# Optimization experiments

Measured on AMD Instinct MI355X. Metric: run time of the kernel, lower is better.

The kernel has to match this reference:

```python
import jax, jax.numpy as jnp
import numpy as np

N_HEADS = 32
N_KV_HEADS = 8
HEAD_DIM = 64  # dim // n_heads = 2048 // 32

def setup_inputs() -> dict:
    key = jax.random.key(0)
    k1, k2, k3, k4, k5 = jax.random.split(key, 5)
    B, T, D = 2, 2048, 2048
    s = 0.02
    return {
        "x": jax.random.normal(k1, (B, T, D), dtype=jnp.float32),
        "wq": jax.random.normal(k2, (D, D), dtype=jnp.float32) * s,
        "wk": jax.random.normal(k3, (N_KV_HEADS * HEAD_DIM, D), dtype=jnp.float32) * s,
        "wv": jax.random.normal(k4, (N_KV_HEADS * HEAD_DIM, D), dtype=jnp.float32) * s,
        "wo": jax.random.normal(k5, (D, D), dtype=jnp.float32) * s,
    }

def reference(x, wq, wk, wv, wo):
    B, T, D = x.shape
    ratio = N_HEADS // N_KV_HEADS
    scale = HEAD_DIM ** -0.5
    # projections (nn.Linear: x @ W.T)
    q = (x @ wq.T).reshape(B, T, N_HEADS, HEAD_DIM)
    k = (x @ wk.T).reshape(B, T, N_KV_HEADS, HEAD_DIM)
    v = (x @ wv.T).reshape(B, T, N_KV_HEADS, HEAD_DIM)
    # GQA expand: [B,T,kvh,d] -> [B,T,kvh*ratio,d]
    k = jnp.broadcast_to(k[:, :, :, None, :], (B, T, N_KV_HEADS, ratio, HEAD_DIM)).reshape(B, T, N_HEADS, HEAD_DIM)
    v = jnp.broadcast_to(v[:, :, :, None, :], (B, T, N_KV_HEADS, ratio, HEAD_DIM)).reshape(B, T, N_HEADS, HEAD_DIM)
    # [B,H,T,d]
    q = q.transpose(0, 2, 1, 3)
    k = k.transpose(0, 2, 1, 3)
    v = v.transpose(0, 2, 1, 3)
    # naive full score matrix [B,H,T,T]
    score = jnp.einsum('bhqd,bhkd->bhqk', q, k) * scale
    causal = jnp.triu(jnp.full((T, T), -jnp.inf, dtype=score.dtype), k=1)
    score = score + causal
    # upcast to fp32 for softmax (matches score.float())
    attn = jax.nn.softmax(score.astype(jnp.float32), axis=-1)
    out = jnp.einsum('bhqk,bhkd->bhqd', attn, v.astype(jnp.float32)).astype(x.dtype)
    out = out.transpose(0, 2, 1, 3).reshape(B, T, N_HEADS * HEAD_DIM)
    return out @ wo.T
```

## Files before the change

### kernel.cpp

```cpp
#include <hip/hip_runtime.h>
#include <hip/hip_bf16.h>

typedef unsigned short u16;
typedef unsigned int   u32;
typedef __attribute__((ext_vector_type(8))) short s16x8;
typedef __attribute__((ext_vector_type(4))) float f32x4;

__device__ __forceinline__ u16 f2bf(float f) {
    u32 u = __float_as_uint(f);
    u += 0x7fff + ((u >> 16) & 1);
    return (u16)(u >> 16);
}

__device__ __forceinline__ u16 f2bf_fast(float f) {
    __hip_bfloat16 h = __float2bfloat16(f);
    return *reinterpret_cast<u16*>(&h);
}

__device__ __forceinline__ f32x4 mfma16(s16x8 a, s16x8 b, f32x4 c) {
    return __builtin_amdgcn_mfma_f32_16x16x32_bf16(a, b, c, 0, 0, 0);
}

#define GLL16(g, l)                                                            \
    __builtin_amdgcn_global_load_lds(                                          \
        (const __attribute__((address_space(1))) void*)(g),                    \
        (__attribute__((address_space(3))) void*)(l), 16, 0, 0)

__global__ void cvt_f32_bf16(const float* __restrict__ src, u16* __restrict__ dst, int n8) {
    int i = blockIdx.x * blockDim.x + threadIdx.x;
    if (i >= n8) return;
    const float4* s4 = reinterpret_cast<const float4*>(src);
    float4 a = s4[2 * i], b = s4[2 * i + 1];
    s16x8 o;
    o[0] = (short)f2bf(a.x); o[1] = (short)f2bf(a.y);
    o[2] = (short)f2bf(a.z); o[3] = (short)f2bf(a.w);
    o[4] = (short)f2bf(b.x); o[5] = (short)f2bf(b.y);
    o[6] = (short)f2bf(b.z); o[7] = (short)f2bf(b.w);
    reinterpret_cast<s16x8*>(dst)[i] = o;
}

__global__ void cvt_weights(const float* __restrict__ wq, const float* __restrict__ wk,
                            const float* __restrict__ wv, const float* __restrict__ wo,
                            u16* __restrict__ wqkv, u16* __restrict__ wob) {
    int i = blockIdx.x * blockDim.x + threadIdx.x;
    const float* src; u16* dst;
    if (i < 524288)       { src = wq + (size_t)i * 8;            dst = wqkv + (size_t)i * 8; }
    else if (i < 655360)  { int j = i - 524288; src = wk + (size_t)j * 8; dst = wqkv + 4194304 + (size_t)j * 8; }
    else if (i < 786432)  { int j = i - 655360; src = wv + (size_t)j * 8; dst = wqkv + 5242880 + (size_t)j * 8; }
    else                  { int j = i - 786432; src = wo + (size_t)j * 8; dst = wob + (size_t)j * 8; }
    const float4* s4 = reinterpret_cast<const float4*>(src);
    float4 a = s4[0], b = s4[1];
    s16x8 o;
    o[0] = (short)f2bf(a.x); o[1] = (short)f2bf(a.y);
    o[2] = (short)f2bf(a.z); o[3] = (short)f2bf(a.w);
    o[4] = (short)f2bf(b.x); o[5] = (short)f2bf(b.y);
    o[6] = (short)f2bf(b.z); o[7] = (short)f2bf(b.w);
    *reinterpret_cast<s16x8*>(dst) = o;
}

template <int BF16_OUT>
__global__ __launch_bounds__(256, 3)
void gemm_bt(const u16* __restrict__ A, const u16* __restrict__ B,
             void* __restrict__ Cout, int M, int N, int K, int nbx) {
    const int nwg = gridDim.x;
    const int cpx = nwg >> 3;
    const int swz = (blockIdx.x & 7) * cpx + (blockIdx.x >> 3);
    const int by = swz / nbx, bx = swz - by * nbx;
    __shared__ __align__(16) u16 As[128 * 32];
    __shared__ __align__(16) u16 Bs[128 * 32];
    const int tid = threadIdx.x;
    const int w = tid >> 6, ln = tid & 63;
    const int m0 = by * 128, n0 = bx * 128;
    const int wr = w >> 1, wc = w & 1;
    const int g = ln >> 4, c15 = ln & 15;
    f32x4 acc[4][4] = {};
    const int srow0 = w * 32 + (ln >> 2);
    const int spos = ln & 3;
    for (int k0 = 0; k0 < K; k0 += 32) {
        __syncthreads();
#pragma unroll
        for (int j = 0; j < 2; ++j) {
            int row = srow0 + j * 16;
            int ch = spos ^ ((row >> 1) & 3);
            const u16* ga = A + (size_t)(m0 + row) * K + k0 + ch * 8;
            GLL16(ga, (char*)As + (w * 32 + j * 16) * 64);
            const u16* gb = B + (size_t)(n0 + row) * K + k0 + ch * 8;
            GLL16(gb, (char*)Bs + (w * 32 + j * 16) * 64);
        }
        __syncthreads();
        s16x8 af[4], bfr[4];
#pragma unroll
        for (int ms = 0; ms < 4; ++ms) {
            int row = wr * 64 + ms * 16 + c15;
            int cp = g ^ ((row >> 1) & 3);
            af[ms] = *reinterpret_cast<const s16x8*>((const char*)As + row * 64 + cp * 16);
        }
#pragma unroll
        for (int ns = 0; ns < 4; ++ns) {
            int row = wc * 64 + ns * 16 + c15;
            int cp = g ^ ((row >> 1) & 3);
            bfr[ns] = *reinterpret_cast<const s16x8*>((const char*)Bs + row * 64 + cp * 16);
        }
        __builtin_amdgcn_s_setprio(1);
#pragma unroll
        for (int ms = 0; ms < 4; ++ms)
#pragma unroll
            for (int ns = 0; ns < 4; ++ns)
                acc[ms][ns] = mfma16(af[ms], bfr[ns], acc[ms][ns]);
        __builtin_amdgcn_s_setprio(0);
    }
#pragma unroll
    for (int ms = 0; ms < 4; ++ms)
#pragma unroll
        for (int ns = 0; ns < 4; ++ns)
#pragma unroll
            for (int r = 0; r < 4; ++r) {
                int row = m0 + wr * 64 + ms * 16 + g * 4 + r;
                int col = n0 + wc * 64 + ns * 16 + c15;
                float v = acc[ms][ns][r];
                if (BF16_OUT)
                    ((u16*)Cout)[(size_t)row * N + col] = f2bf(v);
                else
                    ((float*)Cout)[(size_t)row * N + col] = v;
            }
}

__global__ __launch_bounds__(512, 4)
void attn_fwd(const u16* __restrict__ qkv, u16* __restrict__ outp) {
    const int T = 2048, RS = 3072;
    const int swz = (blockIdx.x & 7) * 64 + (blockIdx.x >> 3);
    const int pr = swz & 31, kvh = (swz >> 5) & 7, b = swz >> 8;
    const int tid = threadIdx.x, w = tid >> 6, ln = tid & 63;
    const int g = ln >> 4, c15 = ln & 15;
    const int h = kvh * 4 + (w >> 1);
    const int qs = w & 1;
    __shared__ __align__(16) u16 Ks[128 * 64];
    __shared__ __align__(16) u16 Vt[64 * 136];
    __shared__ __align__(16) u16 Ps[8][16 * 72];
    const size_t base = (size_t)b * T * RS;
    const float SCALE2 = 0.125f * 1.44269504088896f;
    const float THR = 8.0f;

    for (int ph = 0; ph < 2; ++ph) {
        const int qb = ph ? (63 - pr) : pr;
        const int qg0 = qb * 32 + qs * 16;

        s16x8 qf[2];
#pragma unroll
        for (int ks = 0; ks < 2; ++ks)
            qf[ks] = *reinterpret_cast<const s16x8*>(
                qkv + base + (size_t)(qg0 + c15) * RS + h * 64 + ks * 32 + g * 8);

        f32x4 o[4] = {};
        float mrow[4], lrow[4];
#pragma unroll
        for (int r = 0; r < 4; ++r) { mrow[r] = -INFINITY; lrow[r] = 0.f; }

        const int nt = (qb >> 2) + 1;
        for (int t = 0; t < nt; ++t) {
            __syncthreads();
#pragma unroll
            for (int j = 0; j < 2; ++j) {
                int row = j * 64 + w * 8 + (ln >> 3);
                int ch = (ln & 7) ^ (row & 7);
                const u16* gk = qkv + base + (size_t)(t * 128 + row) * RS + 2048 + kvh * 64 + ch * 8;
                GLL16(gk, (char*)Ks + (j * 64 + w * 8) * 128);
            }
#pragma unroll
            for (int j = 0; j < 2; ++j) {
                int cid = tid + j * 512;
                int kv = cid & 127, dch = cid >> 7;
                s16x8 vv = *reinterpret_cast<const s16x8*>(
                    qkv + base + (size_t)(t * 128 + kv) * RS + 2560 + kvh * 64 + dch * 8);
#pragma unroll
                for (int i = 0; i < 8; ++i)
                    Vt[(dch * 8 + i) * 136 + kv] = (u16)vv[i];
            }
            __syncthreads();

            f32x4 s[8] = {};
#pragma unroll
            for (int ks = 0; ks < 2; ++ks)
#pragma unroll
                for (int nh = 0; nh < 2; ++nh) {
                    s16x8 kf[4];
#pragma unroll
                    for (int n4 = 0; n4 < 4; ++n4) {
                        int row = (nh * 4 + n4) * 16 + c15;
                        int ch = (ks * 4 + g) ^ (row & 7);
                        kf[n4] = *reinterpret_cast<const s16x8*>((const char*)Ks + row * 128 + ch * 16);
                    }
                    __builtin_amdgcn_s_setprio(1);
#pragma unroll
                    for (int n4 = 0; n4 < 4; ++n4)
                        s[nh * 4 + n4] = mfma16(qf[ks], kf[n4], s[nh * 4 + n4]);
                    __builtin_amdgcn_s_setprio(0);
                }

            const bool lastT = (t == nt - 1);
            float mx2[4];
#pragma unroll
            for (int r = 0; r < 4; ++r) {
                float mx = -INFINITY;
                if (lastT) {
                    int qrow = qg0 + g * 4 + r;
#pragma unroll
                    for (int ns = 0; ns < 8; ++ns) {
                        int col = t * 128 + ns * 16 + c15;
                        float v = s[ns][r] * SCALE2;
                        v = (col <= qrow) ? v : -INFINITY;
                        s[ns][r] = v;
                        mx = fmaxf(mx, v);
                    }
                } else {
#pragma unroll
                    for (int ns = 0; ns < 8; ++ns) {
                        float v = s[ns][r] * SCALE2;
                        s[ns][r] = v;
                        mx = fmaxf(mx, v);
                    }
                }
                mx = fmaxf(mx, __shfl_xor(mx, 1));
                mx = fmaxf(mx, __shfl_xor(mx, 2));
                mx = fmaxf(mx, __shfl_xor(mx, 4));
                mx = fmaxf(mx, __shfl_xor(mx, 8));
                mx2[r] = mx;
            }

            float growth = -INFINITY;
#pragma unroll
            for (int r = 0; r < 4; ++r) growth = fmaxf(growth, mx2[r] - mrow[r]);
            if (__any(growth > THR)) {
#pragma unroll
                for (int r = 0; r < 4; ++r) {
                    float mnew = fmaxf(mrow[r], mx2[r]);
                    float fac = exp2f(mrow[r] - mnew);
                    mrow[r] = mnew;
                    lrow[r] *= fac;
#pragma unroll
                    for (int ds = 0; ds < 4; ++ds) o[ds][r] *= fac;
                }
            }

#pragma unroll
            for (int r = 0; r < 4; ++r) {
                float m = mrow[r];
                float rs = 0.f;
#pragma unroll
                for (int ns = 0; ns < 8; ++ns) {
                    float p = exp2f(s[ns][r] - m);
                    s[ns][r] = p;
                    rs += p;
                }
                lrow[r] += rs;
                int prow = g * 4 + r;
#pragma unroll
                for (int ns = 0; ns < 4; ++ns)
                    Ps[w][prow * 72 + ns * 16 + c15] = f2bf_fast(s[ns][r]);
            }
#pragma unroll
            for (int ks = 0; ks < 2; ++ks) {
                s16x8 pf, vf[4];
                pf = *reinterpret_cast<const s16x8*>(&Ps[w][c15 * 72 + ks * 32 + g * 8]);
#pragma unroll
                for (int ds = 0; ds < 4; ++ds)
                    vf[ds] = *reinterpret_cast<const s16x8*>(&Vt[(ds * 16 + c15) * 136 + ks * 32 + g * 8]);
                __builtin_amdgcn_s_setprio(1);
#pragma unroll
                for (int ds = 0; ds < 4; ++ds)
                    o[ds] = mfma16(pf, vf[ds], o[ds]);
                __builtin_amdgcn_s_setprio(0);
            }
#pragma unroll
            for (int r = 0; r < 4; ++r) {
                int prow = g * 4 + r;
#pragma unroll
                for (int ns = 0; ns < 4; ++ns)
                    Ps[w][prow * 72 + ns * 16 + c15] = f2bf_fast(s[ns + 4][r]);
            }
#pragma unroll
            for (int ks = 2; ks < 4; ++ks) {
                s16x8 pf, vf[4];
                pf = *reinterpret_cast<const s16x8*>(&Ps[w][c15 * 72 + (ks - 2) * 32 + g * 8]);
#pragma unroll
                for (int ds = 0; ds < 4; ++ds)
                    vf[ds] = *reinterpret_cast<const s16x8*>(&Vt[(ds * 16 + c15) * 136 + ks * 32 + g * 8]);
                __builtin_amdgcn_s_setprio(1);
#pragma unroll
                for (int ds = 0; ds < 4; ++ds)
                    o[ds] = mfma16(pf, vf[ds], o[ds]);
                __builtin_amdgcn_s_setprio(0);
            }
        }

#pragma unroll
        for (int r = 0; r < 4; ++r) {
            float l = lrow[r];
            l += __shfl_xor(l, 1);
            l += __shfl_xor(l, 2);
            l += __shfl_xor(l, 4);
            l += __shfl_xor(l, 8);
            float inv = 1.0f / l;
            int qrow = qg0 + g * 4 + r;
#pragma unroll
            for (int ds = 0; ds < 4; ++ds)
                outp[(size_t)(b * T + qrow) * 2048 + h * 64 + ds * 16 + c15] =
                    f2bf_fast(o[ds][r] * inv);
        }
    }
}

extern "C" void kernel_launch(void* const* d_in, const int* in_sizes, int n_in,
                              void* d_out, int out_size, void* d_ws, size_t ws_size,
                              hipStream_t stream) {
    const float* x  = (const float*)d_in[0];
    const float* wq = (const float*)d_in[1];
    const float* wk = (const float*)d_in[2];
    const float* wv = (const float*)d_in[3];
    const float* wo = (const float*)d_in[4];

    u16* xb   = (u16*)d_ws;
    u16* wqkv = xb + 8388608;
    u16* wob  = wqkv + 6291456;
    u16* qkvb = wob + 4194304;
    u16* attb = qkvb + 12582912;

    cvt_f32_bf16<<<4096, 256, 0, stream>>>(x, xb, 1048576);
    cvt_weights<<<5120, 256, 0, stream>>>(wq, wk, wv, wo, wqkv, wob);

    gemm_bt<1><<<768, 256, 0, stream>>>(xb, wqkv, qkvb, 4096, 3072, 2048, 24);
    attn_fwd<<<512, 512, 0, stream>>>(qkvb, attb);
    gemm_bt<0><<<512, 256, 0, stream>>>(attb, wob, d_out, 4096, 2048, 2048, 16);
}
```

Before: 314.9 us.

## Double-buffer GEMM and attention K/V tiles and fold softmax scale into Q

The GEMM now double-buffers its A/B shared-memory tiles, so the global-to-LDS load for the next K step is issued before the MFMAs on the current one, and each step needs one barrier instead of two. The attention kernel double-buffers K in LDS and prefetches the next V tile into registers while computing the current tile, with a barrier before the PV stage. The softmax scale times log2(e) is applied to Q in the QKV GEMM epilogue, which removes the per-score multiply in the attention loop. In exchange, attention LDS use grows from about 51 KB to about 67 KB per block, which may cut blocks per CU, and Q is rounded to bf16 after scaling instead of before.

```diff
diff --git a/kernel.cpp b/kernel.cpp
--- a/kernel.cpp
+++ b/kernel.cpp
@@ -61,13 +61,13 @@
 template <int BF16_OUT>
 __global__ __launch_bounds__(256, 3)
 void gemm_bt(const u16* __restrict__ A, const u16* __restrict__ B,
-             void* __restrict__ Cout, int M, int N, int K, int nbx) {
+             void* __restrict__ Cout, int M, int N, int K, int nbx, int qcols) {
     const int nwg = gridDim.x;
     const int cpx = nwg >> 3;
     const int swz = (blockIdx.x & 7) * cpx + (blockIdx.x >> 3);
     const int by = swz / nbx, bx = swz - by * nbx;
-    __shared__ __align__(16) u16 As[128 * 32];
-    __shared__ __align__(16) u16 Bs[128 * 32];
+    __shared__ __align__(16) u16 As[2][128 * 32];
+    __shared__ __align__(16) u16 Bs[2][128 * 32];
     const int tid = threadIdx.x;
     const int w = tid >> 6, ln = tid & 63;
     const int m0 = by * 128, n0 = bx * 128;
@@ -76,30 +76,38 @@
     f32x4 acc[4][4] = {};
     const int srow0 = w * 32 + (ln >> 2);
     const int spos = ln & 3;
-    for (int k0 = 0; k0 < K; k0 += 32) {
-        __syncthreads();
-#pragma unroll
-        for (int j = 0; j < 2; ++j) {
-            int row = srow0 + j * 16;
-            int ch = spos ^ ((row >> 1) & 3);
-            const u16* ga = A + (size_t)(m0 + row) * K + k0 + ch * 8;
-            GLL16(ga, (char*)As + (w * 32 + j * 16) * 64);
-            const u16* gb = B + (size_t)(n0 + row) * K + k0 + ch * 8;
-            GLL16(gb, (char*)Bs + (w * 32 + j * 16) * 64);
-        }
-        __syncthreads();
+    const int nk = K >> 5;
+
+#define GSTAGE(buf, t)                                                          \
+    {                                                                           \
+        _Pragma("unroll")                                                       \
+        for (int j = 0; j < 2; ++j) {                                           \
+            int row = srow0 + j * 16;                                           \
+            int ch = spos ^ ((row >> 1) & 3);                                   \
+            const u16* ga = A + (size_t)(m0 + row) * K + (t) * 32 + ch * 8;     \
+            GLL16(ga, (char*)As[buf] + (w * 32 + j * 16) * 64);                 \
+            const u16* gb = B + (size_t)(n0 + row) * K + (t) * 32 + ch * 8;     \
+            GLL16(gb, (char*)Bs[buf] + (w * 32 + j * 16) * 64);                 \
+        }                                                                       \
+    }
+
+    GSTAGE(0, 0);
+    __syncthreads();
+    for (int t = 0; t < nk; ++t) {
+        const int cur = t & 1;
+        if (t + 1 < nk) GSTAGE(cur ^ 1, t + 1);
         s16x8 af[4], bfr[4];
 #pragma unroll
         for (int ms = 0; ms < 4; ++ms) {
             int row = wr * 64 + ms * 16 + c15;
             int cp = g ^ ((row >> 1) & 3);
-            af[ms] = *reinterpret_cast<const s16x8*>((const char*)As + row * 64 + cp * 16);
+            af[ms] = *reinterpret_cast<const s16x8*>((const char*)As[cur] + row * 64 + cp * 16);
         }
 #pragma unroll
         for (int ns = 0; ns < 4; ++ns) {
             int row = wc * 64 + ns * 16 + c15;
             int cp = g ^ ((row >> 1) & 3);
-            bfr[ns] = *reinterpret_cast<const s16x8*>((const char*)Bs + row * 64 + cp * 16);
+            bfr[ns] = *reinterpret_cast<const s16x8*>((const char*)Bs[cur] + row * 64 + cp * 16);
         }
         __builtin_amdgcn_s_setprio(1);
 #pragma unroll
@@ -108,7 +116,11 @@
             for (int ns = 0; ns < 4; ++ns)
                 acc[ms][ns] = mfma16(af[ms], bfr[ns], acc[ms][ns]);
         __builtin_amdgcn_s_setprio(0);
-    }
+        __syncthreads();
+    }
+#undef GSTAGE
+
+    const float qsc = (n0 < qcols) ? (0.125f * 1.44269504088896f) : 1.0f;
 #pragma unroll
     for (int ms = 0; ms < 4; ++ms)
 #pragma unroll
@@ -119,7 +131,7 @@
                 int col = n0 + wc * 64 + ns * 16 + c15;
                 float v = acc[ms][ns][r];
                 if (BF16_OUT)
-                    ((u16*)Cout)[(size_t)row * N + col] = f2bf(v);
+                    ((u16*)Cout)[(size_t)row * N + col] = f2bf(v * qsc);
                 else
                     ((float*)Cout)[(size_t)row * N + col] = v;
             }
@@ -134,12 +146,43 @@
     const int g = ln >> 4, c15 = ln & 15;
     const int h = kvh * 4 + (w >> 1);
     const int qs = w & 1;
-    __shared__ __align__(16) u16 Ks[128 * 64];
+    __shared__ __align__(16) u16 Ks[2][128 * 64];
     __shared__ __align__(16) u16 Vt[64 * 136];
     __shared__ __align__(16) u16 Ps[8][16 * 72];
     const size_t base = (size_t)b * T * RS;
-    const float SCALE2 = 0.125f * 1.44269504088896f;
     const float THR = 8.0f;
+    const int vkv0 = tid & 127, vdch0 = tid >> 7;
+    const int vkv1 = vkv0, vdch1 = vdch0 + 4;
+
+#define KSTAGE(buf, t)                                                          \
+    {                                                                           \
+        _Pragma("unroll")                                                       \
+        for (int j = 0; j < 2; ++j) {                                           \
+            int row = j * 64 + w * 8 + (ln >> 3);                               \
+            int ch = (ln & 7) ^ (row & 7);                                      \
+            const u16* gk = qkv + base + (size_t)((t) * 128 + row) * RS + 2048  \
+                            + kvh * 64 + ch * 8;                                \
+            GLL16(gk, (char*)Ks[buf] + (j * 64 + w * 8) * 128);                 \
+        }                                                                       \
+    }
+#define VLOAD(t)                                                                \
+    {                                                                           \
+        vv0 = *reinterpret_cast<const s16x8*>(                                  \
+            qkv + base + (size_t)((t) * 128 + vkv0) * RS + 2560                 \
+            + kvh * 64 + vdch0 * 8);                                            \
+        vv1 = *reinterpret_cast<const s16x8*>(                                  \
+            qkv + base + (size_t)((t) * 128 + vkv1) * RS + 2560                 \
+            + kvh * 64 + vdch1 * 8);                                            \
+    }
+#define VWRITE()                                                                \
+    {                                                                           \
+        _Pragma("unroll")                                                       \
+        for (int i = 0; i < 8; ++i)                                             \
+            Vt[(vdch0 * 8 + i) * 136 + vkv0] = (u16)vv0[i];                     \
+        _Pragma("unroll")                                                       \
+        for (int i = 0; i < 8; ++i)                                             \
+            Vt[(vdch1 * 8 + i) * 136 + vkv1] = (u16)vv1[i];                     \
+    }
 
     for (int ph = 0; ph < 2; ++ph) {
         const int qb = ph ? (63 - pr) : pr;
@@ -157,26 +200,22 @@
         for (int r = 0; r < 4; ++r) { mrow[r] = -INFINITY; lrow[r] = 0.f; }
 
         const int nt = (qb >> 2) + 1;
+        s16x8 vv0, vv1;
+        KSTAGE(0, 0);
+        VLOAD(0);
+        __syncthreads();
+
         for (int t = 0; t < nt; ++t) {
-            __syncthreads();
-#pragma unroll
-            for (int j = 0; j < 2; ++j) {
-                int row = j * 64 + w * 8 + (ln >> 3);
-                int ch = (ln & 7) ^ (row & 7);
-                const u16* gk = qkv + base + (size_t)(t * 128 + row) * RS + 2048 + kvh * 64 + ch * 8;
-                GLL16(gk, (char*)Ks + (j * 64 + w * 8) * 128);
-            }
-#pragma unroll
-            for (int j = 0; j < 2; ++j) {
-                int cid = tid + j * 512;
-                int kv = cid & 127, dch = cid >> 7;
-                s16x8 vv = *reinterpret_cast<const s16x8*>(
-                    qkv + base + (size_t)(t * 128 + kv) * RS + 2560 + kvh * 64 + dch * 8);
-#pragma unroll
-                for (int i = 0; i < 8; ++i)
-                    Vt[(dch * 8 + i) * 136 + kv] = (u16)vv[i];
-            }
-            __syncthreads();
+            const int cur = t & 1;
+            VWRITE();
+            s16x8 nv0, nv1;
+            if (t + 1 < nt) {
+                KSTAGE(cur ^ 1, t + 1);
+                nv0 = *reinterpret_cast<const s16x8*>(
+                    qkv + base + (size_t)((t + 1) * 128 + vkv0) * RS + 2560 + kvh * 64 + vdch0 * 8);
+                nv1 = *reinterpret_cast<const s16x8*>(
+                    qkv + base + (size_t)((t + 1) * 128 + vkv1) * RS + 2560 + kvh * 64 + vdch1 * 8);
+            }
 
             f32x4 s[8] = {};
 #pragma unroll
@@ -188,7 +227,8 @@
                     for (int n4 = 0; n4 < 4; ++n4) {
                         int row = (nh * 4 + n4) * 16 + c15;
                         int ch = (ks * 4 + g) ^ (row & 7);
-                        kf[n4] = *reinterpret_cast<const s16x8*>((const char*)Ks + row * 128 + ch * 16);
+                        kf[n4] = *reinterpret_cast<const s16x8*>(
+                            (const char*)Ks[cur] + row * 128 + ch * 16);
                     }
                     __builtin_amdgcn_s_setprio(1);
 #pragma unroll
@@ -207,18 +247,14 @@
 #pragma unroll
                     for (int ns = 0; ns < 8; ++ns) {
                         int col = t * 128 + ns * 16 + c15;
-                        float v = s[ns][r] * SCALE2;
+                        float v = s[ns][r];
                         v = (col <= qrow) ? v : -INFINITY;
                         s[ns][r] = v;
                         mx = fmaxf(mx, v);
                     }
                 } else {
 #pragma unroll
-                    for (int ns = 0; ns < 8; ++ns) {
-                        float v = s[ns][r] * SCALE2;
-                        s[ns][r] = v;
-                        mx = fmaxf(mx, v);
-                    }
+                    for (int ns = 0; ns < 8; ++ns) mx = fmaxf(mx, s[ns][r]);
                 }
                 mx = fmaxf(mx, __shfl_xor(mx, 1));
                 mx = fmaxf(mx, __shfl_xor(mx, 2));
@@ -258,6 +294,11 @@
                 for (int ns = 0; ns < 4; ++ns)
                     Ps[w][prow * 72 + ns * 16 + c15] = f2bf_fast(s[ns][r]);
             }
+
+            asm volatile("s_waitcnt lgkmcnt(0)" ::: "memory");
+            __builtin_amdgcn_s_barrier();
+            __builtin_amdgcn_sched_barrier(0);
+
 #pragma unroll
             for (int ks = 0; ks < 2; ++ks) {
                 s16x8 pf, vf[4];
@@ -291,6 +332,10 @@
                     o[ds] = mfma16(pf, vf[ds], o[ds]);
                 __builtin_amdgcn_s_setprio(0);
             }
+
+            __syncthreads();
+            vv0 = nv0;
+            vv1 = nv1;
         }
 
 #pragma unroll
@@ -308,6 +353,9 @@
                     f2bf_fast(o[ds][r] * inv);
         }
     }
+#undef KSTAGE
+#undef VLOAD
+#undef VWRITE
 }
 
 extern "C" void kernel_launch(void* const* d_in, const int* in_sizes, int n_in,
@@ -328,7 +376,7 @@
     cvt_f32_bf16<<<4096, 256, 0, stream>>>(x, xb, 1048576);
     cvt_weights<<<5120, 256, 0, stream>>>(wq, wk, wv, wo, wqkv, wob);
 
-    gemm_bt<1><<<768, 256, 0, stream>>>(xb, wqkv, qkvb, 4096, 3072, 2048, 24);
+    gemm_bt<1><<<768, 256, 0, stream>>>(xb, wqkv, qkvb, 4096, 3072, 2048, 24, 2048);
     attn_fwd<<<512, 512, 0, stream>>>(qkvb, attb);
-    gemm_bt<0><<<512, 256, 0, stream>>>(attb, wob, d_out, 4096, 2048, 2048, 16);
-}
+    gemm_bt<0><<<512, 256, 0, stream>>>(attb, wob, d_out, 4096, 2048, 2048, 16, 0);
+}
```

Result: no change. 311.8 us (-1.0%).
